# Kernel tuning notes

Measured on AMD Instinct MI355X. Metric: run time of the kernel, lower is better.

## Reference

```python
import jax, jax.numpy as jnp
import numpy as np

B, T, C = 64, 256, 384
H = 6
D = C // H  # head_size = 64


def setup_inputs() -> dict:
    key = jax.random.key(0)
    ks = jax.random.split(key, 6)
    s = 1.0 / np.sqrt(C)
    return {
        "x": jax.random.normal(ks[0], (B, T, C), dtype=jnp.float32),
        "Wk": jax.random.uniform(ks[1], (C, C), jnp.float32, -s, s),
        "Wq": jax.random.uniform(ks[2], (C, C), jnp.float32, -s, s),
        "Wv": jax.random.uniform(ks[3], (C, C), jnp.float32, -s, s),
        "Wo": jax.random.uniform(ks[4], (C, C), jnp.float32, -s, s),
        "bo": jax.random.uniform(ks[5], (C,), jnp.float32, -s, s),
    }


def reference(x, Wk, Wq, Wv, Wo, bo):
    b, t, c = x.shape
    # QKV projections (no bias), split heads: [B, H, T, D]
    k = (x @ Wk.T).reshape(b, t, H, D).transpose(0, 2, 1, 3)
    q = (x @ Wq.T).reshape(b, t, H, D).transpose(0, 2, 1, 3)
    v = (x @ Wv.T).reshape(b, t, H, D).transpose(0, 2, 1, 3)
    # Scores scaled by C**-0.5 (as in the original module, not head_size**-0.5)
    wei = jnp.einsum("bhqd,bhkd->bhqk", q, k) * (c ** -0.5)
    mask = jnp.tril(jnp.ones((t, t), dtype=bool))
    wei = jnp.where(mask, wei, -jnp.inf)
    wei = jax.nn.softmax(wei, axis=-1)
    out = jnp.einsum("bhqk,bhkd->bhqd", wei, v)
    out = out.transpose(0, 2, 1, 3).reshape(b, t, c)
    # Output projection (dropout is identity at inference)
    return out @ Wo.T + bo
```

## Files before the change

### kernel.cpp

```cpp
#include <hip/hip_runtime.h>
#include <hip/hip_bf16.h>

typedef unsigned short u16;
typedef __attribute__((ext_vector_type(8))) short short8;
typedef __attribute__((ext_vector_type(4))) float f32x4;

#define BATCH 64
#define SEQ   256
#define CDIM  384
#define NHEAD 6
#define DHEAD 64
#define NROW  16384

constexpr float SCALE = 0.051031036307982884f;

__device__ __forceinline__ f32x4 mfma16(short8 a, short8 b, f32x4 c) {
    return __builtin_amdgcn_mfma_f32_16x16x32_bf16(a, b, c, 0, 0, 0);
}

__device__ __forceinline__ u16 f2b(float f) {
    __hip_bfloat16 h = __float2bfloat16(f);
    return *reinterpret_cast<u16*>(&h);
}

__device__ __forceinline__ void gload_lds16(const u16* g, u16* l) {
    __builtin_amdgcn_global_load_lds(
        (const __attribute__((address_space(1))) void*)g,
        (__attribute__((address_space(3))) void*)l, 16, 0, 0);
}

__global__ __launch_bounds__(256) void cvt_all(
        const float* __restrict__ x,
        const float* __restrict__ Wk, const float* __restrict__ Wq,
        const float* __restrict__ Wv, const float* __restrict__ Wo,
        u16* __restrict__ xb,
        u16* __restrict__ wkb, u16* __restrict__ wqb,
        u16* __restrict__ wvb, u16* __restrict__ wob)
{
    int blk = blockIdx.x;
    const float* s;
    u16* d;
    if (blk < 3072) {
        s = x; d = xb;
    } else {
        const int w = blk - 3072;
        const int z = w / 72;
        blk = w - z * 72;
        s = (z == 0) ? Wk : (z == 1) ? Wq : (z == 2) ? Wv : Wo;
        d = (z == 0) ? wkb : (z == 1) ? wqb : (z == 2) ? wvb : wob;
    }
    const int i = (blk * 256 + (int)threadIdx.x) * 8;
    const float4 a = *(const float4*)(s + i);
    const float4 b = *(const float4*)(s + i + 4);
    short8 r;
    r[0] = (short)f2b(a.x); r[1] = (short)f2b(a.y);
    r[2] = (short)f2b(a.z); r[3] = (short)f2b(a.w);
    r[4] = (short)f2b(b.x); r[5] = (short)f2b(b.y);
    r[6] = (short)f2b(b.z); r[7] = (short)f2b(b.w);
    *(short8*)(d + i) = r;
}

__global__ __launch_bounds__(256) void gemm_qkv(
        const u16* __restrict__ X, const u16* __restrict__ Wk,
        const u16* __restrict__ Wv, const u16* __restrict__ Wq,
        u16* __restrict__ Kd, u16* __restrict__ VTd, u16* __restrict__ Qd)
{
    __shared__ u16 SMEM[32768];

    const int bid   = blockIdx.x;
    const int xcd   = bid & 7;
    const int i     = bid >> 3;
    const int igrp  = i / 9;
    const int j     = i - igrp * 9;
    const int panel = xcd * 16 + igrp;
    const int m0    = panel * 128;
    const int n0    = (j % 3) * 128;
    const int z     = j / 3;
    const u16* W = (z == 0) ? Wk : (z == 1 ? Wv : Wq);

    const int tid  = threadIdx.x;
    const int lane = tid & 63;
    const int wv   = tid >> 6;
    const int l15  = lane & 15;
    const int q4   = lane >> 4;
    const int wm   = (wv >> 1) * 64;
    const int wn   = (wv & 1) * 64;

    f32x4 acc[4][4] = {};

    auto STAGE = [&](int kk, int buf) {
#pragma unroll
        for (int ch = 0; ch < 4; ++ch) {
            const int f  = (ch * 256 + tid) * 8;
            const int r  = f >> 6;
            const int cb = (f ^ ((r & 7) << 3)) & 63;
            const int lb = buf * 16384 + (ch * 256 + wv * 64) * 8;
            gload_lds16(X + (size_t)(m0 + r) * CDIM + kk + cb, SMEM + lb);
            gload_lds16(W + (size_t)(n0 + r) * CDIM + kk + cb, SMEM + 8192 + lb);
        }
    };

    STAGE(0, 0);
#pragma unroll
    for (int t = 0; t < 6; ++t) {
        const int cur = t & 1;
        if (t < 5) {
            STAGE((t + 1) * 64, cur ^ 1);
            asm volatile("s_waitcnt vmcnt(8)" ::: "memory");
        } else {
            asm volatile("s_waitcnt vmcnt(0)" ::: "memory");
        }
        asm volatile("s_barrier" ::: "memory");

        const u16* As = SMEM + cur * 16384;
        const u16* Bs = SMEM + cur * 16384 + 8192;
#pragma unroll
        for (int ks = 0; ks < 2; ++ks) {
            short8 af[4], bf[4];
#pragma unroll
            for (int tt = 0; tt < 4; ++tt) {
                const int ra = wm + tt * 16 + l15;
                const int rb = wn + tt * 16 + l15;
                af[tt] = *(const short8*)(As + ra * 64 +
                        ((ks * 32 + q4 * 8) ^ ((ra & 7) << 3)));
                bf[tt] = *(const short8*)(Bs + rb * 64 +
                        ((ks * 32 + q4 * 8) ^ ((rb & 7) << 3)));
            }
#pragma unroll
            for (int tm = 0; tm < 4; ++tm)
#pragma unroll
                for (int tn = 0; tn < 4; ++tn)
                    acc[tm][tn] = mfma16(af[tm], bf[tn], acc[tm][tn]);
        }
        asm volatile("s_barrier" ::: "memory");
    }

    if (z != 1) {
        u16* D = (z == 0) ? Kd : Qd;
        u16* T = SMEM;
#pragma unroll
        for (int tm = 0; tm < 4; ++tm)
#pragma unroll
            for (int tn = 0; tn < 4; ++tn) {
                const int cl = wn + tn * 16 + l15;
#pragma unroll
                for (int r = 0; r < 4; ++r) {
                    const int row = wm + tm * 16 + q4 * 4 + r;
                    T[row * 128 + (((cl >> 3) ^ (row & 7)) << 3) + (cl & 7)] =
                        f2b(acc[tm][tn][r]);
                }
            }
        __syncthreads();
        const int seg0 = tid >> 3;
        const int c    = tid & 7;
#pragma unroll
        for (int it = 0; it < 8; ++it) {
            const int S   = it * 32 + seg0;
            const int row = S >> 1;
            const int hf  = S & 1;
            const int rowg = m0 + row;
            const int b  = rowg >> 8, tt = rowg & 255;
            const int h  = (n0 + hf * 64) >> 6;
            const int chunk = (hf * 8 + c) ^ (row & 7);
            *(uint4*)(D + (size_t)((b * NHEAD + h) * SEQ + tt) * DHEAD + c * 8) =
                *(const uint4*)(T + row * 128 + chunk * 8);
        }
    } else {
        u16* T = SMEM;
#pragma unroll
        for (int tm = 0; tm < 4; ++tm)
#pragma unroll
            for (int tn = 0; tn < 4; ++tn) {
                const int cl = wn + tn * 16 + l15;
#pragma unroll
                for (int r = 0; r < 4; ++r) {
                    const int rl = wm + tm * 16 + q4 * 4 + r;
                    T[cl * 136 + rl] = f2b(acc[tm][tn][r]);
                }
            }
        __syncthreads();
        const int b  = m0 >> 8;
        const int t0 = m0 & 255;
        const int fl = tid >> 1;
        const int hf = tid & 1;
        const int fg = n0 + fl;
        const int h  = fg >> 6, d = fg & 63;
        u16* dst = VTd + ((size_t)(b * NHEAD + h) * DHEAD + d) * SEQ + t0 + hf * 64;
        const u16* src = T + fl * 136 + hf * 64;
#pragma unroll
        for (int j2 = 0; j2 < 8; ++j2)
            *(uint4*)(dst + j2 * 8) = *(const uint4*)(src + j2 * 8);
    }
}

#define PLD 264

template <int CH>
__device__ __forceinline__ void attn_body(
        const u16* __restrict__ Qg, const u16* __restrict__ Kg,
        const u16* __restrict__ VTg, u16* __restrict__ Og, int bh,
        u16* SA, u16* Pbase)
{
    constexpr int NKEY = 64 * (CH + 1);
    constexpr int KT   = NKEY / 16;
    constexpr int NPH  = (NKEY + 127) / 128;

    const int tid  = threadIdx.x;
    const int wv   = tid >> 6;
    const int lane = tid & 63;
    const int l15  = lane & 15;
    const int q4   = lane >> 4;
    const int qrow0 = CH * 64 + wv * 16;
    const int qmax  = qrow0 + 15;
    u16* Pl = Pbase + wv * 16 * PLD;

    short8 aq[2];
#pragma unroll
    for (int ks = 0; ks < 2; ++ks)
        aq[ks] = *(const short8*)(Qg + (size_t)(bh * SEQ + qrow0 + l15) * DHEAD
                                     + ks * 32 + q4 * 8);

    u16* Kbuf = SA;
    f32x4 s[KT];
#pragma unroll
    for (int ph = 0; ph < NPH; ++ph) {
        const int rows = (NKEY - ph * 128) < 128 ? (NKEY - ph * 128) : 128;
        for (int it = 0; it < rows / 32; ++it) {
            const int r  = it * 32 + (tid >> 3);
            const int d0 = (tid & 7) * 8;
            *(uint4*)(Kbuf + r * 72 + d0) =
                *(const uint4*)(Kg + (size_t)(bh * SEQ + ph * 128 + r) * DHEAD + d0);
        }
        __syncthreads();
#pragma unroll
        for (int t = 0; t < rows / 16; ++t) {
            const int gt = ph * 8 + t;
            if (gt * 16 <= qmax) {
                f32x4 z = {0.f, 0.f, 0.f, 0.f};
#pragma unroll
                for (int ks = 0; ks < 2; ++ks) {
                    short8 bk = *(const short8*)(Kbuf + (t * 16 + l15) * 72
                                                 + ks * 32 + q4 * 8);
                    z = mfma16(aq[ks], bk, z);
                }
                const int kc = gt * 16 + l15;
#pragma unroll
                for (int r = 0; r < 4; ++r) {
                    float v = z[r] * SCALE;
                    if (kc > qrow0 + q4 * 4 + r) v = -1e30f;
                    z[r] = v;
                }
                s[gt] = z;
            } else {
                f32x4 neg = {-1e30f, -1e30f, -1e30f, -1e30f};
                s[gt] = neg;
            }
        }
        __syncthreads();
    }

    float mx[4], sm[4], rs[4];
#pragma unroll
    for (int r = 0; r < 4; ++r) {
        float m = -1e30f;
#pragma unroll
        for (int t = 0; t < KT; ++t) m = fmaxf(m, s[t][r]);
#pragma unroll
        for (int off = 1; off < 16; off <<= 1)
            m = fmaxf(m, __shfl_xor(m, off, 16));
        mx[r] = m;
        sm[r] = 0.f;
    }
#pragma unroll
    for (int t = 0; t < KT; ++t)
#pragma unroll
        for (int r = 0; r < 4; ++r) {
            float p = __expf(s[t][r] - mx[r]);
            s[t][r] = p;
            sm[r] += p;
        }
#pragma unroll
    for (int r = 0; r < 4; ++r) {
#pragma unroll
        for (int off = 1; off < 16; off <<= 1)
            sm[r] += __shfl_xor(sm[r], off, 16);
        rs[r] = 1.f / sm[r];
    }

#pragma unroll
    for (int gt = 0; gt < KT; ++gt)
#pragma unroll
        for (int r = 0; r < 4; ++r)
            Pl[(q4 * 4 + r) * PLD + gt * 16 + l15] = f2b(s[gt][r]);

    u16* Vt = SA;
    f32x4 o[4] = {};
#pragma unroll
    for (int ph = 0; ph < NPH; ++ph) {
        const int rows = (NKEY - ph * 128) < 128 ? (NKEY - ph * 128) : 128;
        const int cpr  = rows >> 3;
#pragma unroll
        for (int it = 0; it < 4; ++it) {
            if (it < cpr / 4) {
                const int flat = it * 256 + tid;
                const int rd = flat / cpr;
                const int kc = (flat - rd * cpr) * 8;
                *(uint4*)(Vt + rd * 136 + kc) =
                    *(const uint4*)(VTg + ((size_t)bh * DHEAD + rd) * SEQ
                                        + ph * 128 + kc);
            }
        }
        __syncthreads();
#pragma unroll
        for (int ks = 0; ks < rows / 32; ++ks) {
            const int gks = ph * 4 + ks;
            if (gks * 32 <= qmax) {
                short8 ap = *(const short8*)(Pl + l15 * PLD + gks * 32 + q4 * 8);
#pragma unroll
                for (int tn = 0; tn < 4; ++tn) {
                    short8 bv = *(const short8*)(Vt + (tn * 16 + l15) * 136
                                                 + ks * 32 + q4 * 8);
                    o[tn] = mfma16(ap, bv, o[tn]);
                }
            }
        }
        __syncthreads();
    }

    u16* OL = SA;
#pragma unroll
    for (int tn = 0; tn < 4; ++tn) {
        const int col = tn * 16 + l15;
#pragma unroll
        for (int r = 0; r < 4; ++r) {
            const int row = wv * 16 + q4 * 4 + r;
            OL[row * 64 + (((col >> 3) ^ (row & 7)) << 3) + (col & 7)] =
                f2b(o[tn][r] * rs[r]);
        }
    }
    __syncthreads();
    const int b  = bh / NHEAD;
    const int h  = bh - b * NHEAD;
    const int seg0 = tid >> 3;
    const int c    = tid & 7;
#pragma unroll
    for (int it = 0; it < 2; ++it) {
        const int row = it * 32 + seg0;
        const int chunk = c ^ (row & 7);
        *(uint4*)(Og + (size_t)(b * SEQ + CH * 64 + row) * CDIM
                     + h * DHEAD + c * 8) =
            *(const uint4*)(OL + row * 64 + chunk * 8);
    }
}

__global__ __launch_bounds__(256) void attn_kernel(
        const u16* __restrict__ Qg, const u16* __restrict__ Kg,
        const u16* __restrict__ VTg, u16* __restrict__ Og)
{
    __shared__ u16 SA[128 * 72];
    __shared__ u16 Pls[4 * 16 * PLD];
    const int bid = blockIdx.x;
    const int xcd = bid & 7;
    const int g   = bid >> 3;
    const int bh  = xcd * 48 + (g >> 2);
    const int ch  = g & 3;
    switch (ch) {
        case 0: attn_body<0>(Qg, Kg, VTg, Og, bh, SA, Pls); break;
        case 1: attn_body<1>(Qg, Kg, VTg, Og, bh, SA, Pls); break;
        case 2: attn_body<2>(Qg, Kg, VTg, Og, bh, SA, Pls); break;
        default: attn_body<3>(Qg, Kg, VTg, Og, bh, SA, Pls); break;
    }
}

__global__ __launch_bounds__(256) void gemm_out(
        const u16* __restrict__ O, const u16* __restrict__ Wo,
        const float* __restrict__ bias, float* __restrict__ out)
{
    __shared__ u16 As[64 * 64];
    __shared__ u16 Bs[128 * 64];

    const int bid = blockIdx.x;
    const int xcd = bid & 7;
    const int g   = bid >> 3;
    const int mt  = xcd * 32 + g / 3;
    const int n0  = (g % 3) * 128;
    const int m0  = mt * 64;

    const int tid  = threadIdx.x;
    const int lane = tid & 63;
    const int wv   = tid >> 6;
    const int l15  = lane & 15;
    const int q4   = lane >> 4;
    const int wm   = (wv >> 1) * 32;
    const int wn   = (wv & 1) * 64;

    f32x4 acc[2][4] = {};

    for (int kk = 0; kk < CDIM; kk += 64) {
        __syncthreads();
#pragma unroll
        for (int ch = 0; ch < 4; ++ch) {
            const int f = (ch * 256 + tid) * 8;
            const int r = f >> 6;
            const int c = (f ^ ((r & 7) << 3)) & 63;
            const int lb = (ch * 256 + wv * 64) * 8;
            gload_lds16(Wo + (size_t)(n0 + r) * CDIM + kk + c, Bs + lb);
            if (ch < 2)
                gload_lds16(O + (size_t)(m0 + r) * CDIM + kk + c, As + lb);
        }
        __syncthreads();

#pragma unroll
        for (int ks = 0; ks < 2; ++ks) {
            short8 af[2], bf[4];
#pragma unroll
            for (int t = 0; t < 2; ++t) {
                const int ra = wm + t * 16 + l15;
                af[t] = *(const short8*)(As + ra * 64 +
                        ((ks * 32 + q4 * 8) ^ ((ra & 7) << 3)));
            }
#pragma unroll
            for (int t = 0; t < 4; ++t) {
                const int rb = wn + t * 16 + l15;
                bf[t] = *(const short8*)(Bs + rb * 64 +
                        ((ks * 32 + q4 * 8) ^ ((rb & 7) << 3)));
            }
#pragma unroll
            for (int tm = 0; tm < 2; ++tm)
#pragma unroll
                for (int tn = 0; tn < 4; ++tn)
                    acc[tm][tn] = mfma16(af[tm], bf[tn], acc[tm][tn]);
        }
    }

#pragma unroll
    for (int tm = 0; tm < 2; ++tm) {
#pragma unroll
        for (int tn = 0; tn < 4; ++tn) {
            const int col = n0 + wn + tn * 16 + l15;
            const float bb = bias[col];
#pragma unroll
            for (int r = 0; r < 4; ++r) {
                const int row = m0 + wm + tm * 16 + q4 * 4 + r;
                out[(size_t)row * CDIM + col] = acc[tm][tn][r] + bb;
            }
        }
    }
}

extern "C" void kernel_launch(void* const* d_in, const int* in_sizes, int n_in,
                              void* d_out, int out_size, void* d_ws, size_t ws_size,
                              hipStream_t stream)
{
    const float* x  = (const float*)d_in[0];
    const float* Wk = (const float*)d_in[1];
    const float* Wq = (const float*)d_in[2];
    const float* Wv = (const float*)d_in[3];
    const float* Wo = (const float*)d_in[4];
    const float* bo = (const float*)d_in[5];
    float* out = (float*)d_out;

    const size_t SZ = (size_t)NROW * CDIM;
    const size_t WZ = (size_t)CDIM * CDIM;
    u16* xb  = (u16*)d_ws;
    u16* Wkb = xb  + SZ;
    u16* Wqb = Wkb + WZ;
    u16* Wvb = Wqb + WZ;
    u16* Wob = Wvb + WZ;
    u16* Kw  = Wob + WZ;
    u16* Qw  = Kw + SZ;
    u16* Ow  = Qw + SZ;
    u16* VTw = (u16*)d_out;

    cvt_all<<<dim3(3360), 256, 0, stream>>>(
        x, Wk, Wq, Wv, Wo, xb, Wkb, Wqb, Wvb, Wob);

    gemm_qkv<<<dim3(1152), 256, 0, stream>>>(xb, Wkb, Wvb, Wqb, Kw, VTw, Qw);

    attn_kernel<<<dim3(1536), 256, 0, stream>>>(Qw, Kw, VTw, Ow);

    gemm_out<<<dim3(768), 256, 0, stream>>>(Ow, Wob, bo, out);
}
```

Measured before the change: 143.5 us.

## Prefetch K/V tiles into registers in attention and double-buffer output GEMM

In the attention kernel, the second 128-key chunk of K and V is loaded into registers while the first chunk is being computed. The first V chunk is also prefetched before the softmax, so global load latency overlaps with MFMA and softmax work. The output projection GEMM moves to a two-stage LDS double buffer with explicit vmcnt waits and raw s_barriers, so the next K-slice loads while the current one is multiplied. The cost is more registers (up to eight uint4 staging slots) and twice the LDS in the GEMM, which may lower occupancy; the hand-written waitcnt/barrier sequence is also fragile.

```diff
diff --git a/kernel.cpp b/kernel.cpp
--- a/kernel.cpp
+++ b/kernel.cpp
@@ -204,6 +204,8 @@
     constexpr int NKEY = 64 * (CH + 1);
     constexpr int KT   = NKEY / 16;
     constexpr int NPH  = (NKEY + 127) / 128;
+    constexpr int R0   = (NKEY < 128) ? NKEY : 128;
+    constexpr int R1   = NKEY - R0;
 
     const int tid  = threadIdx.x;
     const int wv   = tid >> 6;
@@ -222,19 +224,61 @@
 
     u16* Kbuf = SA;
     f32x4 s[KT];
-#pragma unroll
-    for (int ph = 0; ph < NPH; ++ph) {
-        const int rows = (NKEY - ph * 128) < 128 ? (NKEY - ph * 128) : 128;
-        for (int it = 0; it < rows / 32; ++it) {
-            const int r  = it * 32 + (tid >> 3);
-            const int d0 = (tid & 7) * 8;
-            *(uint4*)(Kbuf + r * 72 + d0) =
-                *(const uint4*)(Kg + (size_t)(bh * SEQ + ph * 128 + r) * DHEAD + d0);
-        }
+    const int kr = tid >> 3;
+    const int kd = (tid & 7) * 8;
+
+#pragma unroll
+    for (int it = 0; it < R0 / 32; ++it) {
+        const int r = it * 32 + kr;
+        *(uint4*)(Kbuf + r * 72 + kd) =
+            *(const uint4*)(Kg + (size_t)(bh * SEQ + r) * DHEAD + kd);
+    }
+    uint4 kpre[4];
+    if constexpr (NPH == 2) {
+#pragma unroll
+        for (int it = 0; it < R1 / 32; ++it) {
+            const int r = it * 32 + kr;
+            kpre[it] = *(const uint4*)(Kg + (size_t)(bh * SEQ + 128 + r) * DHEAD + kd);
+        }
+    }
+    __syncthreads();
+
+#pragma unroll
+    for (int t = 0; t < R0 / 16; ++t) {
+        const int gt = t;
+        if (gt * 16 <= qmax) {
+            f32x4 z = {0.f, 0.f, 0.f, 0.f};
+#pragma unroll
+            for (int ks = 0; ks < 2; ++ks) {
+                short8 bk = *(const short8*)(Kbuf + (t * 16 + l15) * 72
+                                             + ks * 32 + q4 * 8);
+                z = mfma16(aq[ks], bk, z);
+            }
+            const int kc = gt * 16 + l15;
+#pragma unroll
+            for (int r = 0; r < 4; ++r) {
+                float v = z[r] * SCALE;
+                if (kc > qrow0 + q4 * 4 + r) v = -1e30f;
+                z[r] = v;
+            }
+            s[gt] = z;
+        } else {
+            f32x4 neg = {-1e30f, -1e30f, -1e30f, -1e30f};
+            s[gt] = neg;
+        }
+    }
+
+    if constexpr (NPH == 2) {
         __syncthreads();
 #pragma unroll
-        for (int t = 0; t < rows / 16; ++t) {
-            const int gt = ph * 8 + t;
+        for (int it = 0; it < R1 / 32; ++it) {
+            const int r = it * 32 + kr;
+            *(uint4*)(Kbuf + r * 72 + kd) = kpre[it];
+        }
+        __syncthreads();
+#pragma unroll
+        for (int t = 0; t < R1 / 16; ++t) {
+            const int gt = 8 + t;
             if (gt * 16 <= qmax) {
                 f32x4 z = {0.f, 0.f, 0.f, 0.f};
 #pragma unroll
@@ -256,7 +300,18 @@
                 s[gt] = neg;
             }
         }
-        __syncthreads();
+    }
+    __syncthreads();
+
+    constexpr int C0  = R0 >> 3;
+    constexpr int NV0 = (64 * C0) / 256;
+    uint4 va[4];
+#pragma unroll
+    for (int it = 0; it < NV0; ++it) {
+        const int flat = it * 256 + tid;
+        const int rd = flat / C0;
+        const int kc = (flat - rd * C0) * 8;
+        va[it] = *(const uint4*)(VTg + ((size_t)bh * DHEAD + rd) * SEQ + kc);
     }
 
     float mx[4], sm[4], rs[4];
@@ -294,26 +349,55 @@
             Pl[(q4 * 4 + r) * PLD + gt * 16 + l15] = f2b(s[gt][r]);
 
     u16* Vt = SA;
+#pragma unroll
+    for (int it = 0; it < NV0; ++it) {
+        const int flat = it * 256 + tid;
+        const int rd = flat / C0;
+        const int kc = (flat - rd * C0) * 8;
+        *(uint4*)(Vt + rd * 136 + kc) = va[it];
+    }
+    constexpr int C1  = (R1 > 0) ? (R1 >> 3) : 8;
+    constexpr int NV1 = (R1 > 0) ? (64 * (R1 >> 3)) / 256 : 0;
+    uint4 vb[4];
+    if constexpr (NPH == 2) {
+#pragma unroll
+        for (int it = 0; it < NV1; ++it) {
+            const int flat = it * 256 + tid;
+            const int rd = flat / C1;
+            const int kc = (flat - rd * C1) * 8;
+            vb[it] = *(const uint4*)(VTg + ((size_t)bh * DHEAD + rd) * SEQ
+                                         + 128 + kc);
+        }
+    }
+    __syncthreads();
+
     f32x4 o[4] = {};
 #pragma unroll
-    for (int ph = 0; ph < NPH; ++ph) {
-        const int rows = (NKEY - ph * 128) < 128 ? (NKEY - ph * 128) : 128;
-        const int cpr  = rows >> 3;
-#pragma unroll
-        for (int it = 0; it < 4; ++it) {
-            if (it < cpr / 4) {
-                const int flat = it * 256 + tid;
-                const int rd = flat / cpr;
-                const int kc = (flat - rd * cpr) * 8;
-                *(uint4*)(Vt + rd * 136 + kc) =
-                    *(const uint4*)(VTg + ((size_t)bh * DHEAD + rd) * SEQ
-                                        + ph * 128 + kc);
-            }
-        }
+    for (int ks = 0; ks < R0 / 32; ++ks) {
+        const int gks = ks;
+        if (gks * 32 <= qmax) {
+            short8 ap = *(const short8*)(Pl + l15 * PLD + gks * 32 + q4 * 8);
+#pragma unroll
+            for (int tn = 0; tn < 4; ++tn) {
+                short8 bv = *(const short8*)(Vt + (tn * 16 + l15) * 136
+                                             + ks * 32 + q4 * 8);
+                o[tn] = mfma16(ap, bv, o[tn]);
+            }
+        }
+    }
+    if constexpr (NPH == 2) {
         __syncthreads();
 #pragma unroll
-        for (int ks = 0; ks < rows / 32; ++ks) {
-            const int gks = ph * 4 + ks;
+        for (int it = 0; it < NV1; ++it) {
+            const int flat = it * 256 + tid;
+            const int rd = flat / C1;
+            const int kc = (flat - rd * C1) * 8;
+            *(uint4*)(Vt + rd * 136 + kc) = vb[it];
+        }
+        __syncthreads();
+#pragma unroll
+        for (int ks = 0; ks < R1 / 32; ++ks) {
+            const int gks = 4 + ks;
             if (gks * 32 <= qmax) {
                 short8 ap = *(const short8*)(Pl + l15 * PLD + gks * 32 + q4 * 8);
 #pragma unroll
@@ -324,8 +408,8 @@
                 }
             }
         }
-        __syncthreads();
-    }
+    }
+    __syncthreads();
 
     u16* OL = SA;
 #pragma unroll
@@ -376,8 +460,7 @@
         const u16* __restrict__ O, const u16* __restrict__ Wo,
         const float* __restrict__ bias, float* __restrict__ out)
 {
-    __shared__ u16 As[64 * 64];
-    __shared__ u16 Bs[128 * 64];
+    __shared__ u16 SMEM[24576];
 
     const int bid = blockIdx.x;
     const int xcd = bid & 7;
@@ -396,33 +479,48 @@
 
     f32x4 acc[2][4] = {};
 
-    for (int kk = 0; kk < CDIM; kk += 64) {
-        __syncthreads();
+    auto STAGE = [&](int kk, int buf) {
 #pragma unroll
         for (int ch = 0; ch < 4; ++ch) {
             const int f = (ch * 256 + tid) * 8;
             const int r = f >> 6;
             const int c = (f ^ ((r & 7) << 3)) & 63;
             const int lb = (ch * 256 + wv * 64) * 8;
-            gload_lds16(Wo + (size_t)(n0 + r) * CDIM + kk + c, Bs + lb);
+            gload_lds16(Wo + (size_t)(n0 + r) * CDIM + kk + c,
+                        SMEM + buf * 12288 + 4096 + lb);
             if (ch < 2)
-                gload_lds16(O + (size_t)(m0 + r) * CDIM + kk + c, As + lb);
-        }
-        __syncthreads();
-
+                gload_lds16(O + (size_t)(m0 + r) * CDIM + kk + c,
+                            SMEM + buf * 12288 + lb);
+        }
+    };
+
+    STAGE(0, 0);
+#pragma unroll
+    for (int t = 0; t < 6; ++t) {
+        const int cur = t & 1;
+        if (t < 5) {
+            STAGE((t + 1) * 64, cur ^ 1);
+            asm volatile("s_waitcnt vmcnt(6)" ::: "memory");
+        } else {
+            asm volatile("s_waitcnt vmcnt(0)" ::: "memory");
+        }
+        asm volatile("s_barrier" ::: "memory");
+
+        const u16* As = SMEM + cur * 12288;
+        const u16* Bs = SMEM + cur * 12288 + 4096;
 #pragma unroll
         for (int ks = 0; ks < 2; ++ks) {
             short8 af[2], bf[4];
 #pragma unroll
-            for (int t = 0; t < 2; ++t) {
-                const int ra = wm + t * 16 + l15;
-                af[t] = *(const short8*)(As + ra * 64 +
+            for (int tt = 0; tt < 2; ++tt) {
+                const int ra = wm + tt * 16 + l15;
+                af[tt] = *(const short8*)(As + ra * 64 +
                         ((ks * 32 + q4 * 8) ^ ((ra & 7) << 3)));
             }
 #pragma unroll
-            for (int t = 0; t < 4; ++t) {
-                const int rb = wn + t * 16 + l15;
-                bf[t] = *(const short8*)(Bs + rb * 64 +
+            for (int tt = 0; tt < 4; ++tt) {
+                const int rb = wn + tt * 16 + l15;
+                bf[tt] = *(const short8*)(Bs + rb * 64 +
                         ((ks * 32 + q4 * 8) ^ ((rb & 7) << 3)));
             }
 #pragma unroll
@@ -431,6 +529,7 @@
                 for (int tn = 0; tn < 4; ++tn)
                     acc[tm][tn] = mfma16(af[tm], bf[tn], acc[tm][tn]);
         }
+        asm volatile("s_barrier" ::: "memory");
     }
 
 #pragma unroll
```

Result: slower. 150.6 us (+4.9%).

## Stage softmax probabilities in halves to shrink LDS and raise attention occupancy

Applied to the files above, without the earlier changes.

The attention kernel now writes the bf16 probability tile into LDS 128 keys at a time, reusing a half-size buffer (stride 136 instead of 264) between the two key phases. The first V tile load is interleaved with the P store so one barrier covers both. A min-blocks-per-CU hint of 4 is added to launch bounds. The goal is lower shared memory per block so more blocks fit per CU, at the cost of an extra barrier and possible register pressure from the launch-bounds constraint.

```diff
diff --git a/kernel.cpp b/kernel.cpp
--- a/kernel.cpp
+++ b/kernel.cpp
@@ -193,7 +193,7 @@
     }
 }
 
-#define PLD 264
+#define PLD 136
 
 template <int CH>
 __device__ __forceinline__ void attn_body(
@@ -204,6 +204,8 @@
     constexpr int NKEY = 64 * (CH + 1);
     constexpr int KT   = NKEY / 16;
     constexpr int NPH  = (NKEY + 127) / 128;
+    constexpr int R0   = (NKEY < 128) ? NKEY : 128;
+    constexpr int R1   = NKEY - R0;
 
     const int tid  = threadIdx.x;
     const int wv   = tid >> 6;
@@ -287,35 +289,63 @@
         rs[r] = 1.f / sm[r];
     }
 
-#pragma unroll
-    for (int gt = 0; gt < KT; ++gt)
+    u16* Vt = SA;
+    f32x4 o[4] = {};
+
+    constexpr int C0  = R0 >> 3;
+    constexpr int NV0 = (64 * C0) / 256;
+#pragma unroll
+    for (int it = 0; it < NV0; ++it) {
+        const int flat = it * 256 + tid;
+        const int rd = flat / C0;
+        const int kc = (flat - rd * C0) * 8;
+        *(uint4*)(Vt + rd * 136 + kc) =
+            *(const uint4*)(VTg + ((size_t)bh * DHEAD + rd) * SEQ + kc);
+    }
+#pragma unroll
+    for (int gt = 0; gt < R0 / 16; ++gt)
 #pragma unroll
         for (int r = 0; r < 4; ++r)
             Pl[(q4 * 4 + r) * PLD + gt * 16 + l15] = f2b(s[gt][r]);
-
-    u16* Vt = SA;
-    f32x4 o[4] = {};
-#pragma unroll
-    for (int ph = 0; ph < NPH; ++ph) {
-        const int rows = (NKEY - ph * 128) < 128 ? (NKEY - ph * 128) : 128;
-        const int cpr  = rows >> 3;
-#pragma unroll
-        for (int it = 0; it < 4; ++it) {
-            if (it < cpr / 4) {
-                const int flat = it * 256 + tid;
-                const int rd = flat / cpr;
-                const int kc = (flat - rd * cpr) * 8;
-                *(uint4*)(Vt + rd * 136 + kc) =
-                    *(const uint4*)(VTg + ((size_t)bh * DHEAD + rd) * SEQ
-                                        + ph * 128 + kc);
-            }
-        }
-        __syncthreads();
-#pragma unroll
-        for (int ks = 0; ks < rows / 32; ++ks) {
-            const int gks = ph * 4 + ks;
+    __syncthreads();
+
+#pragma unroll
+    for (int ks = 0; ks < R0 / 32; ++ks) {
+        if (ks * 32 <= qmax) {
+            short8 ap = *(const short8*)(Pl + l15 * PLD + ks * 32 + q4 * 8);
+#pragma unroll
+            for (int tn = 0; tn < 4; ++tn) {
+                short8 bv = *(const short8*)(Vt + (tn * 16 + l15) * 136
+                                             + ks * 32 + q4 * 8);
+                o[tn] = mfma16(ap, bv, o[tn]);
+            }
+        }
+    }
+
+    if constexpr (NPH == 2) {
+        __syncthreads();
+        constexpr int C1  = R1 >> 3;
+        constexpr int NV1 = (64 * C1) / 256;
+#pragma unroll
+        for (int it = 0; it < NV1; ++it) {
+            const int flat = it * 256 + tid;
+            const int rd = flat / C1;
+            const int kc = (flat - rd * C1) * 8;
+            *(uint4*)(Vt + rd * 136 + kc) =
+                *(const uint4*)(VTg + ((size_t)bh * DHEAD + rd) * SEQ + 128 + kc);
+        }
+#pragma unroll
+        for (int gt = 8; gt < KT; ++gt)
+#pragma unroll
+            for (int r = 0; r < 4; ++r)
+                Pl[(q4 * 4 + r) * PLD + (gt - 8) * 16 + l15] = f2b(s[gt][r]);
+        __syncthreads();
+
+#pragma unroll
+        for (int ks = 0; ks < R1 / 32; ++ks) {
+            const int gks = 4 + ks;
             if (gks * 32 <= qmax) {
-                short8 ap = *(const short8*)(Pl + l15 * PLD + gks * 32 + q4 * 8);
+                short8 ap = *(const short8*)(Pl + l15 * PLD + ks * 32 + q4 * 8);
 #pragma unroll
                 for (int tn = 0; tn < 4; ++tn) {
                     short8 bv = *(const short8*)(Vt + (tn * 16 + l15) * 136
@@ -324,8 +354,8 @@
                 }
             }
         }
-        __syncthreads();
-    }
+    }
+    __syncthreads();
 
     u16* OL = SA;
 #pragma unroll
@@ -353,7 +383,7 @@
     }
 }
 
-__global__ __launch_bounds__(256) void attn_kernel(
+__global__ __launch_bounds__(256, 4) void attn_kernel(
         const u16* __restrict__ Qg, const u16* __restrict__ Kg,
         const u16* __restrict__ VTg, u16* __restrict__ Og)
 {
```

Measured after the change: 137.2 us. 1.05x faster.
